# Optimization experiments

Measured on AMD Instinct MI355X. Metric: run time of the kernel, lower is better.

The kernel has to match this reference:

```python
import jax, jax.numpy as jnp
import numpy as np

N, C_IN, C_OUT, H, W = 8, 128, 64, 128, 128
KH, KW, DILATE = 9, 9, 2


def _shifted(xp, dh, dw, dilate, Hh, Ww):
    # xp: zero-padded [N,C,H+2ph,W+2pw]; returns window-offset (dh,dw) view [N,C,H,W]
    return xp[:, :, dh * dilate:dh * dilate + Hh, dw * dilate:dw * dilate + Ww]


def local_similar(q, k, kH, kW, dilate):
    # q,k: [N,C,H,W] -> logits [N,H,W,kH*kW]
    n, c, h, w = q.shape
    ph, pw = dilate * (kH // 2), dilate * (kW // 2)
    kp = jnp.pad(k, ((0, 0), (0, 0), (ph, ph), (pw, pw)))
    outs = []
    for dh in range(kH):
        for dw in range(kW):
            ks = _shifted(kp, dh, dw, dilate, h, w)
            outs.append(jnp.einsum('nchw,nchw->nhw', q, ks))
    return jnp.stack(outs, axis=-1)


def local_weighting(v, wgt, kH, kW, dilate):
    # v: [N,C,H,W], wgt: [N,H,W,kH*kW] -> [N,C,H,W]
    n, c, h, w = v.shape
    ph, pw = dilate * (kH // 2), dilate * (kW // 2)
    vp = jnp.pad(v, ((0, 0), (0, 0), (ph, ph), (pw, pw)))
    out = jnp.zeros_like(v)
    idx = 0
    for dh in range(kH):
        for dw in range(kW):
            vs = _shifted(vp, dh, dw, dilate, h, w)
            out = out + vs * wgt[..., idx][:, None, :, :]
            idx += 1
    return out


def setup_inputs() -> dict:
    key = jax.random.key(0)
    kx, k1, k2, k3 = jax.random.split(key, 4)
    s = 1.0 / np.sqrt(C_IN)
    return {
        'x': jax.random.normal(kx, (N, C_IN, H, W), dtype=jnp.float32),
        'W1': jax.random.normal(k1, (C_OUT, C_IN), dtype=jnp.float32) * s,
        'W2': jax.random.normal(k2, (C_OUT, C_IN), dtype=jnp.float32) * s,
        'W3': jax.random.normal(k3, (C_OUT, C_IN), dtype=jnp.float32) * s,
    }


def reference(x, W1, W2, W3):
    # 1x1 convs (no bias)
    x1 = jnp.einsum('oc,nchw->nohw', W1, x)
    x2 = jnp.einsum('oc,nchw->nohw', W2, x)
    x3 = jnp.einsum('oc,nchw->nohw', W3, x)
    logits = local_similar(x1, x2, KH, KW, DILATE)      # [N,H,W,kH*kW]
    weight = jax.nn.softmax(logits, axis=-1)
    out = local_weighting(x3, weight, KH, KW, DILATE)   # [N,C_out,H,W]
    return out
```

## Files before the change

### kernel.cpp

```cpp
#include <hip/hip_runtime.h>
#include <hip/hip_bf16.h>
#include <cstdint>
#include <cstddef>

#define NB   8
#define CIN  128
#define COUT 64
#define HH   128
#define WWD  128
#define NPIX (NB*HH*WWD)
#define PLANE NPIX
#define LOG2E 1.44269504088896340736f

typedef _Float16 f16;
typedef _Float16 half4_t __attribute__((ext_vector_type(4)));
typedef _Float16 half8_t __attribute__((ext_vector_type(8)));
typedef float    float4_t __attribute__((ext_vector_type(4)));

__global__ __launch_bounds__(256) void wsetup_k(
    const float* __restrict__ W1, const float* __restrict__ W2,
    const float* __restrict__ W3, f16* __restrict__ Wf)
{
  int idx = blockIdx.x * 256 + threadIdx.x;
  int mat = idx >> 13;
  int rem = idx & 8191;
  const float* src = (mat == 0 ? W1 : (mat == 1 ? W2 : W3));
  float v = src[rem];
  if (mat == 0) v *= LOG2E;
  Wf[idx] = (f16)v;
}

__global__ __launch_bounds__(256, 4) void conv_mfma_k(
    const float* __restrict__ x, const f16* __restrict__ Wf,
    f16* __restrict__ Qi, f16* __restrict__ Ki, f16* __restrict__ V2)
{
  __shared__ __align__(16) f16 xs[64 * 136];

  int tid = threadIdx.x, lane = tid & 63, wv = tid >> 6;
  int pxt = blockIdx.x * 64;
  int n = pxt >> 14, hwt = pxt & 16383;

  {
    const float* xp = x + ((size_t)(n * CIN + wv * 32) << 14) + hwt + lane;
    #pragma unroll
    for (int c0 = 0; c0 < 32; c0 += 8) {
      half8_t hh;
      #pragma unroll
      for (int j = 0; j < 8; ++j)
        hh[j] = (f16)xp[(size_t)(c0 + j) << 14];
      *(half8_t*)&xs[lane * 136 + wv * 32 + c0] = hh;
    }
  }
  __syncthreads();

  int l15 = lane & 15, q4 = lane >> 4;

  half8_t wq[4], wk[4], wvf[4];
  #pragma unroll
  for (int k0 = 0; k0 < 4; ++k0) {
    wq[k0]  = *(const half8_t*)&Wf[((wv     )*16 + l15)*128 + k0*32 + q4*8];
    wk[k0]  = *(const half8_t*)&Wf[((wv +  4)*16 + l15)*128 + k0*32 + q4*8];
    wvf[k0] = *(const half8_t*)&Wf[((wv +  8)*16 + l15)*128 + k0*32 + q4*8];
  }

  #pragma unroll
  for (int mt = 0; mt < 4; ++mt) {
    float4_t cq = {0.f,0.f,0.f,0.f}, ck = {0.f,0.f,0.f,0.f}, cv = {0.f,0.f,0.f,0.f};
    #pragma unroll
    for (int k0 = 0; k0 < 4; ++k0) {
      half8_t xa = *(half8_t*)&xs[(mt*16 + l15)*136 + k0*32 + q4*8];
      cq = __builtin_amdgcn_mfma_f32_16x16x32_f16(wq[k0],  xa, cq, 0, 0, 0);
      ck = __builtin_amdgcn_mfma_f32_16x16x32_f16(wk[k0],  xa, ck, 0, 0, 0);
      cv = __builtin_amdgcn_mfma_f32_16x16x32_f16(xa, wvf[k0], cv, 0, 0, 0);
    }
    int pxq = pxt + mt*16 + l15;
    int g   = wv*2 + (q4 >> 1);
    half4_t hq = {(f16)cq[0], (f16)cq[1], (f16)cq[2], (f16)cq[3]};
    half4_t hk = {(f16)ck[0], (f16)ck[1], (f16)ck[2], (f16)ck[3]};
    *(half4_t*)&Qi[((size_t)g * PLANE + pxq) * 8 + (q4 & 1)*4] = hq;
    *(half4_t*)&Ki[((size_t)g * PLANE + pxq) * 8 + (q4 & 1)*4] = hk;
    half4_t hv = {(f16)cv[0], (f16)cv[1], (f16)cv[2], (f16)cv[3]};
    *(half4_t*)&V2[(size_t)(wv*16 + l15) * PLANE + pxt + mt*16 + q4*4] = hv;
  }
}

__global__ __launch_bounds__(512, 4) void attn_fused_k(
    const f16* __restrict__ Qi, const f16* __restrict__ Ki,
    const f16* __restrict__ V2, float* __restrict__ out)
{
  __shared__ __align__(16) f16 plds[8][2][16 * 40];

  int tid = threadIdx.x, lane = tid & 63, wv = tid >> 6;
  int l15 = lane & 15, q4 = lane >> 4;
  int b = blockIdx.x;
  int n = b & 7;
  int p = b >> 3;
  int h0 = (p >> 1)*4 + (p & 1);
  int h2 = h0 + 2;
  int seg = wv * 16;
  int nb = n << 14;

  f16* P0 = &plds[wv][0][0];
  f16* P1 = &plds[wv][1][0];

  half8_t aq0[2], aq1[2];
  {
    int px0 = nb + (h0 << 7) + seg + l15;
    aq0[0] = *(const half8_t*)&Qi[((size_t)(q4    ) * PLANE + px0) * 8];
    aq0[1] = *(const half8_t*)&Qi[((size_t)(q4 + 4) * PLANE + px0) * 8];
    int px1 = px0 + 256;
    aq1[0] = *(const half8_t*)&Qi[((size_t)(q4    ) * PLANE + px1) * 8];
    aq1[1] = *(const half8_t*)&Qi[((size_t)(q4 + 4) * PLANE + px1) * 8];
  }

  unsigned vbits = 0;
  #pragma unroll
  for (int jt = 0; jt < 2; ++jt)
    #pragma unroll
    for (int r = 0; r < 4; ++r) {
      int jw = seg - 8 + jt*16 + q4*4 + r;
      int iw = seg + l15;
      int d  = jw - iw;
      bool val = (((d & 1) == 0) & (d >= -8) & (d <= 8) & ((unsigned)jw < 128u));
      vbits |= ((unsigned)val) << (jt*4 + r);
    }

  float m0 = -1e30f, s0 = 0.f, m1 = -1e30f, s1 = 0.f;
  float4_t o0[4], o1[4];
  #pragma unroll
  for (int ct = 0; ct < 4; ++ct) {
    o0[ct] = (float4_t){0.f,0.f,0.f,0.f};
    o1[ct] = (float4_t){0.f,0.f,0.f,0.f};
  }

  auto row_body = [&](const half8_t* aq, float& m, float& l,
                      float4_t* o, f16* P, const half8_t (&bk)[2][2],
                      const half8_t (&bv)[4]) {
    float4_t st0 = (float4_t){0.f,0.f,0.f,0.f};
    float4_t st1 = (float4_t){0.f,0.f,0.f,0.f};
    st0 = __builtin_amdgcn_mfma_f32_16x16x32_f16(bk[0][0], aq[0], st0, 0, 0, 0);
    st0 = __builtin_amdgcn_mfma_f32_16x16x32_f16(bk[0][1], aq[1], st0, 0, 0, 0);
    st1 = __builtin_amdgcn_mfma_f32_16x16x32_f16(bk[1][0], aq[0], st1, 0, 0, 0);
    st1 = __builtin_amdgcn_mfma_f32_16x16x32_f16(bk[1][1], aq[1], st1, 0, 0, 0);
    #pragma unroll
    for (int r = 0; r < 4; ++r) {
      st0[r] = ((vbits >> r)       & 1u) ? st0[r] : -1e30f;
      st1[r] = ((vbits >> (4 + r)) & 1u) ? st1[r] : -1e30f;
    }
    float v = fmaxf(fmaxf(fmaxf(st0[0], st0[1]), fmaxf(st0[2], st0[3])),
                    fmaxf(fmaxf(st1[0], st1[1]), fmaxf(st1[2], st1[3])));
    v = fmaxf(v, __shfl_xor(v, 16, 64));
    v = fmaxf(v, __shfl_xor(v, 32, 64));
    float mn = fmaxf(m, v);
    float al = exp2f(m - mn);
    m = mn;
    #pragma unroll
    for (int r = 0; r < 4; ++r) {
      st0[r] = exp2f(st0[r] - mn);
      st1[r] = exp2f(st1[r] - mn);
    }
    float rs = (st0[0] + st0[1]) + (st0[2] + st0[3])
             + (st1[0] + st1[1]) + (st1[2] + st1[3]);
    rs += __shfl_xor(rs, 16, 64);
    rs += __shfl_xor(rs, 32, 64);
    l = l * al + rs;
    float4_t alv;
    #pragma unroll
    for (int r = 0; r < 4; ++r) alv[r] = __shfl(al, q4*4 + r, 64);
    #pragma unroll
    for (int ct = 0; ct < 4; ++ct)
      #pragma unroll
      for (int r = 0; r < 4; ++r) o[ct][r] *= alv[r];
    half4_t p0 = {(f16)st0[0], (f16)st0[1], (f16)st0[2], (f16)st0[3]};
    half4_t p1 = {(f16)st1[0], (f16)st1[1], (f16)st1[2], (f16)st1[3]};
    *(half4_t*)&P[l15*40      + q4*4] = p0;
    *(half4_t*)&P[l15*40 + 16 + q4*4] = p1;
    half8_t ap = *(half8_t*)&P[l15*40 + q4*8];
    #pragma unroll
    for (int ct = 0; ct < 4; ++ct)
      o[ct] = __builtin_amdgcn_mfma_f32_16x16x32_f16(ap, bv[ct], o[ct], 0, 0, 0);
  };

  for (int hs = h0 - 8; hs <= h0 + 10; hs += 2) {
    if (hs < 0 || hs > 127) continue;
    bool a0 = (hs <= h0 + 8);
    bool a1 = (hs >= h0 - 6);
    int jbase = nb + (hs << 7) + seg - 8;

    half8_t bk[2][2];
    #pragma unroll
    for (int jt = 0; jt < 2; ++jt) {
      int pxj = jbase + jt*16 + l15;
      bk[jt][0] = *(const half8_t*)&Ki[((size_t)(q4    ) * PLANE + pxj) * 8];
      bk[jt][1] = *(const half8_t*)&Ki[((size_t)(q4 + 4) * PLANE + pxj) * 8];
    }
    half8_t bv[4];
    #pragma unroll
    for (int ct = 0; ct < 4; ++ct)
      bv[ct] = *(const half8_t*)&V2[(size_t)(ct*16 + l15) * PLANE + jbase + q4*8];

    if (a0) row_body(aq0, m0, s0, o0, P0, bk, bv);
    if (a1) row_body(aq1, m1, s1, o1, P1, bk, bv);
  }

  int iw = seg + l15;
  int wlo = iw - 8; if (wlo < 0) wlo = 0;
  int whi = iw + 8; if (whi > 127) whi = 127;
  int vw = ((whi - wlo) >> 1) + 1;
  #pragma unroll
  for (int row = 0; row < 2; ++row) {
    int hr = row ? h2 : h0;
    int hlo = hr - 8; if (hlo < 0) hlo = 0;
    int hhi = hr + 8; if (hhi > 127) hhi = 127;
    int vh = ((hhi - hlo) >> 1) + 1;
    float cnt = (float)(81 - vh * vw);
    float m = row ? m1 : m0, l = row ? s1 : s0;
    float mn = fmaxf(m, 0.f);
    float em = exp2f(m - mn);
    float sc = em / (l * em + cnt * exp2f(-mn));
    float4_t scv;
    #pragma unroll
    for (int r = 0; r < 4; ++r) scv[r] = __shfl(sc, q4*4 + r, 64);
    const float4_t* o = row ? o1 : o0;
    #pragma unroll
    for (int ct = 0; ct < 4; ++ct) {
      size_t ob = ((size_t)(n*COUT + ct*16 + l15) << 14) + (hr << 7) + seg + q4*4;
      float4_t stv;
      #pragma unroll
      for (int r = 0; r < 4; ++r) stv[r] = o[ct][r] * scv[r];
      *(float4_t*)&out[ob] = stv;
    }
  }
}

extern "C" void kernel_launch(void* const* d_in, const int* in_sizes, int n_in,
                              void* d_out, int out_size, void* d_ws, size_t ws_size,
                              hipStream_t stream)
{
  const float* x  = (const float*)d_in[0];
  const float* W1 = (const float*)d_in[1];
  const float* W2 = (const float*)d_in[2];
  const float* W3 = (const float*)d_in[3];

  f16* Wf = (f16*)d_ws;
  f16* Qi = Wf + (size_t)192 * 128;
  f16* Ki = Qi + (size_t)8 * PLANE * 8;
  f16* V2 = Ki + (size_t)8 * PLANE * 8;

  float* outp = (float*)d_out;

  wsetup_k    <<<96,       256, 0, stream>>>(W1, W2, W3, Wf);
  conv_mfma_k <<<NPIX/64,  256, 0, stream>>>(x, Wf, Qi, Ki, V2);
  attn_fused_k<<<NB*HH/2,  512, 0, stream>>>(Qi, Ki, V2, outp);
}
```

Measured before the change: 159.0 us.

## Fuse weight setup into conv, double-buffer K/V loads, split attention blocks

Removes the separate weight conversion kernel; each conv block now reads the fp32 weights and converts them to fp16 in registers, overlapping that with the x tile load. The attention kernel moves from 512-thread to 256-thread blocks covering half a row width each, which doubles the grid to 1024 blocks. It also double-buffers the K/V row loads so the next row's loads are issued before the current row's MFMA and softmax work. Conv blocks are remapped so consecutive blocks interleave images. The cost is redundant weight conversion in every conv block, more register pressure from the double buffers, and a lower occupancy hint.

```diff
diff --git a/kernel.cpp b/kernel.cpp
--- a/kernel.cpp
+++ b/kernel.cpp
@@ -6,9 +6,7 @@
 #define NB   8
 #define CIN  128
 #define COUT 64
-#define HH   128
-#define WWD  128
-#define NPIX (NB*HH*WWD)
+#define NPIX 131072
 #define PLANE NPIX
 #define LOG2E 1.44269504088896340736f
 
@@ -17,28 +15,18 @@
 typedef _Float16 half8_t __attribute__((ext_vector_type(8)));
 typedef float    float4_t __attribute__((ext_vector_type(4)));
 
-__global__ __launch_bounds__(256) void wsetup_k(
-    const float* __restrict__ W1, const float* __restrict__ W2,
-    const float* __restrict__ W3, f16* __restrict__ Wf)
-{
-  int idx = blockIdx.x * 256 + threadIdx.x;
-  int mat = idx >> 13;
-  int rem = idx & 8191;
-  const float* src = (mat == 0 ? W1 : (mat == 1 ? W2 : W3));
-  float v = src[rem];
-  if (mat == 0) v *= LOG2E;
-  Wf[idx] = (f16)v;
-}
-
 __global__ __launch_bounds__(256, 4) void conv_mfma_k(
-    const float* __restrict__ x, const f16* __restrict__ Wf,
+    const float* __restrict__ x,  const float* __restrict__ W1,
+    const float* __restrict__ W2, const float* __restrict__ W3,
     f16* __restrict__ Qi, f16* __restrict__ Ki, f16* __restrict__ V2)
 {
   __shared__ __align__(16) f16 xs[64 * 136];
 
   int tid = threadIdx.x, lane = tid & 63, wv = tid >> 6;
-  int pxt = blockIdx.x * 64;
-  int n = pxt >> 14, hwt = pxt & 16383;
+  int b = blockIdx.x;
+  int n = b & 7, t = b >> 3;
+  int pxt = (n << 14) + t * 64;
+  int hwt = pxt & 16383;
 
   {
     const float* xp = x + ((size_t)(n * CIN + wv * 32) << 14) + hwt + lane;
@@ -51,17 +39,25 @@
       *(half8_t*)&xs[lane * 136 + wv * 32 + c0] = hh;
     }
   }
+
+  int l15 = lane & 15, q4 = lane >> 4;
+
+  half8_t wq[4], wk[4], wvf[4];
+  {
+    const float* r1 = W1 + (wv*16 + l15)*128 + q4*8;
+    const float* r2 = W2 + (wv*16 + l15)*128 + q4*8;
+    const float* r3 = W3 + (wv*16 + l15)*128 + q4*8;
+    #pragma unroll
+    for (int k0 = 0; k0 < 4; ++k0) {
+      #pragma unroll
+      for (int j = 0; j < 8; ++j) {
+        wq[k0][j]  = (f16)(r1[k0*32 + j] * LOG2E);
+        wk[k0][j]  = (f16)(r2[k0*32 + j]);
+        wvf[k0][j] = (f16)(r3[k0*32 + j]);
+      }
+    }
+  }
   __syncthreads();
-
-  int l15 = lane & 15, q4 = lane >> 4;
-
-  half8_t wq[4], wk[4], wvf[4];
-  #pragma unroll
-  for (int k0 = 0; k0 < 4; ++k0) {
-    wq[k0]  = *(const half8_t*)&Wf[((wv     )*16 + l15)*128 + k0*32 + q4*8];
-    wk[k0]  = *(const half8_t*)&Wf[((wv +  4)*16 + l15)*128 + k0*32 + q4*8];
-    wvf[k0] = *(const half8_t*)&Wf[((wv +  8)*16 + l15)*128 + k0*32 + q4*8];
-  }
 
   #pragma unroll
   for (int mt = 0; mt < 4; ++mt) {
@@ -84,20 +80,21 @@
   }
 }
 
-__global__ __launch_bounds__(512, 4) void attn_fused_k(
+__global__ __launch_bounds__(256, 3) void attn_fused_k(
     const f16* __restrict__ Qi, const f16* __restrict__ Ki,
     const f16* __restrict__ V2, float* __restrict__ out)
 {
-  __shared__ __align__(16) f16 plds[8][2][16 * 40];
+  __shared__ __align__(16) f16 plds[4][2][16 * 40];
 
   int tid = threadIdx.x, lane = tid & 63, wv = tid >> 6;
   int l15 = lane & 15, q4 = lane >> 4;
   int b = blockIdx.x;
   int n = b & 7;
-  int p = b >> 3;
+  int r = b >> 3;
+  int p = r & 63, hseg = r >> 6;
   int h0 = (p >> 1)*4 + (p & 1);
   int h2 = h0 + 2;
-  int seg = wv * 16;
+  int seg = (hseg*4 + wv) * 16;
   int nb = n << 14;
 
   f16* P0 = &plds[wv][0][0];
@@ -117,12 +114,12 @@
   #pragma unroll
   for (int jt = 0; jt < 2; ++jt)
     #pragma unroll
-    for (int r = 0; r < 4; ++r) {
-      int jw = seg - 8 + jt*16 + q4*4 + r;
+    for (int rr = 0; rr < 4; ++rr) {
+      int jw = seg - 8 + jt*16 + q4*4 + rr;
       int iw = seg + l15;
       int d  = jw - iw;
       bool val = (((d & 1) == 0) & (d >= -8) & (d <= 8) & ((unsigned)jw < 128u));
-      vbits |= ((unsigned)val) << (jt*4 + r);
+      vbits |= ((unsigned)val) << (jt*4 + rr);
     }
 
   float m0 = -1e30f, s0 = 0.f, m1 = -1e30f, s1 = 0.f;
@@ -143,9 +140,9 @@
     st1 = __builtin_amdgcn_mfma_f32_16x16x32_f16(bk[1][0], aq[0], st1, 0, 0, 0);
     st1 = __builtin_amdgcn_mfma_f32_16x16x32_f16(bk[1][1], aq[1], st1, 0, 0, 0);
     #pragma unroll
-    for (int r = 0; r < 4; ++r) {
-      st0[r] = ((vbits >> r)       & 1u) ? st0[r] : -1e30f;
-      st1[r] = ((vbits >> (4 + r)) & 1u) ? st1[r] : -1e30f;
+    for (int rr = 0; rr < 4; ++rr) {
+      st0[rr] = ((vbits >> rr)       & 1u) ? st0[rr] : -1e30f;
+      st1[rr] = ((vbits >> (4 + rr)) & 1u) ? st1[rr] : -1e30f;
     }
     float v = fmaxf(fmaxf(fmaxf(st0[0], st0[1]), fmaxf(st0[2], st0[3])),
                     fmaxf(fmaxf(st1[0], st1[1]), fmaxf(st1[2], st1[3])));
@@ -155,9 +152,9 @@
     float al = exp2f(m - mn);
     m = mn;
     #pragma unroll
-    for (int r = 0; r < 4; ++r) {
-      st0[r] = exp2f(st0[r] - mn);
-      st1[r] = exp2f(st1[r] - mn);
+    for (int rr = 0; rr < 4; ++rr) {
+      st0[rr] = exp2f(st0[rr] - mn);
+      st1[rr] = exp2f(st1[rr] - mn);
     }
     float rs = (st0[0] + st0[1]) + (st0[2] + st0[3])
              + (st1[0] + st1[1]) + (st1[2] + st1[3]);
@@ -166,11 +163,11 @@
     l = l * al + rs;
     float4_t alv;
     #pragma unroll
-    for (int r = 0; r < 4; ++r) alv[r] = __shfl(al, q4*4 + r, 64);
+    for (int rr = 0; rr < 4; ++rr) alv[rr] = __shfl(al, q4*4 + rr, 64);
     #pragma unroll
     for (int ct = 0; ct < 4; ++ct)
       #pragma unroll
-      for (int r = 0; r < 4; ++r) o[ct][r] *= alv[r];
+      for (int rr = 0; rr < 4; ++rr) o[ct][rr] *= alv[rr];
     half4_t p0 = {(f16)st0[0], (f16)st0[1], (f16)st0[2], (f16)st0[3]};
     half4_t p1 = {(f16)st1[0], (f16)st1[1], (f16)st1[2], (f16)st1[3]};
     *(half4_t*)&P[l15*40      + q4*4] = p0;
@@ -181,26 +178,37 @@
       o[ct] = __builtin_amdgcn_mfma_f32_16x16x32_f16(ap, bv[ct], o[ct], 0, 0, 0);
   };
 
-  for (int hs = h0 - 8; hs <= h0 + 10; hs += 2) {
-    if (hs < 0 || hs > 127) continue;
-    bool a0 = (hs <= h0 + 8);
-    bool a1 = (hs >= h0 - 6);
+  auto loadKV = [&](int hs, half8_t (&bk)[2][2], half8_t (&bv)[4]) {
     int jbase = nb + (hs << 7) + seg - 8;
-
-    half8_t bk[2][2];
     #pragma unroll
     for (int jt = 0; jt < 2; ++jt) {
       int pxj = jbase + jt*16 + l15;
       bk[jt][0] = *(const half8_t*)&Ki[((size_t)(q4    ) * PLANE + pxj) * 8];
       bk[jt][1] = *(const half8_t*)&Ki[((size_t)(q4 + 4) * PLANE + pxj) * 8];
     }
-    half8_t bv[4];
     #pragma unroll
     for (int ct = 0; ct < 4; ++ct)
       bv[ct] = *(const half8_t*)&V2[(size_t)(ct*16 + l15) * PLANE + jbase + q4*8];
-
-    if (a0) row_body(aq0, m0, s0, o0, P0, bk, bv);
-    if (a1) row_body(aq1, m1, s1, o1, P1, bk, bv);
+  };
+
+  auto process = [&](int hs, const half8_t (&bk)[2][2], const half8_t (&bv)[4]) {
+    if (hs <= h0 + 8) row_body(aq0, m0, s0, o0, P0, bk, bv);
+    if (hs >= h2 - 8) row_body(aq1, m1, s1, o1, P1, bk, bv);
+  };
+
+  int hs_lo = h0 - 8;  if (hs_lo < 0)   hs_lo = h0 & 1;
+  int hs_hi = h0 + 10; if (hs_hi > 127) hs_hi = 126 + (h0 & 1);
+
+  half8_t bkA[2][2], bvA[4], bkB[2][2], bvB[4];
+  loadKV(hs_lo, bkA, bvA);
+  int hs = hs_lo;
+  while (true) {
+    if (hs + 2 <= hs_hi) loadKV(hs + 2, bkB, bvB);
+    process(hs, bkA, bvA);
+    hs += 2; if (hs > hs_hi) break;
+    if (hs + 2 <= hs_hi) loadKV(hs + 2, bkA, bvA);
+    process(hs, bkB, bvB);
+    hs += 2; if (hs > hs_hi) break;
   }
 
   int iw = seg + l15;
@@ -220,14 +228,14 @@
     float sc = em / (l * em + cnt * exp2f(-mn));
     float4_t scv;
     #pragma unroll
-    for (int r = 0; r < 4; ++r) scv[r] = __shfl(sc, q4*4 + r, 64);
+    for (int rr = 0; rr < 4; ++rr) scv[rr] = __shfl(sc, q4*4 + rr, 64);
     const float4_t* o = row ? o1 : o0;
     #pragma unroll
     for (int ct = 0; ct < 4; ++ct) {
       size_t ob = ((size_t)(n*COUT + ct*16 + l15) << 14) + (hr << 7) + seg + q4*4;
       float4_t stv;
       #pragma unroll
-      for (int r = 0; r < 4; ++r) stv[r] = o[ct][r] * scv[r];
+      for (int rr = 0; rr < 4; ++rr) stv[rr] = o[ct][rr] * scv[rr];
       *(float4_t*)&out[ob] = stv;
     }
   }
@@ -242,14 +250,12 @@
   const float* W2 = (const float*)d_in[2];
   const float* W3 = (const float*)d_in[3];
 
-  f16* Wf = (f16*)d_ws;
-  f16* Qi = Wf + (size_t)192 * 128;
+  f16* Qi = (f16*)d_ws + 2048;
   f16* Ki = Qi + (size_t)8 * PLANE * 8;
   f16* V2 = Ki + (size_t)8 * PLANE * 8;
 
   float* outp = (float*)d_out;
 
-  wsetup_k    <<<96,       256, 0, stream>>>(W1, W2, W3, Wf);
-  conv_mfma_k <<<NPIX/64,  256, 0, stream>>>(x, Wf, Qi, Ki, V2);
-  attn_fused_k<<<NB*HH/2,  512, 0, stream>>>(Qi, Ki, V2, outp);
+  conv_mfma_k <<<NPIX/64, 256, 0, stream>>>(x, W1, W2, W3, Qi, Ki, V2);
+  attn_fused_k<<<1024,    256, 0, stream>>>(Qi, Ki, V2, outp);
 }
```

New measurement: 176.0 us. 10.7% more time.

## Drop online-softmax max tracking and switch P and V to bf16 MFMA

Applied to the files above, without the earlier changes.

Removes the running-max and rescale steps of the online softmax. Raw logits are exponentiated directly, and each lane keeps a partial row sum that is shuffle-reduced once at the end. P and V are stored as bf16, with P truncated from the fp32 bits, so the unshifted exponentials fit in bf16's fp32-like exponent range, and the PV product uses the bf16 MFMA. This cuts per-tile shuffles, max reductions and accumulator rescaling. In exchange it can overflow if logits ever exceed about 128 in log2 units, and it loses mantissa precision in P and V.

```diff
diff --git a/kernel.cpp b/kernel.cpp
--- a/kernel.cpp
+++ b/kernel.cpp
@@ -6,16 +6,21 @@
 #define NB   8
 #define CIN  128
 #define COUT 64
-#define HH   128
-#define WWD  128
-#define NPIX (NB*HH*WWD)
+#define NPIX 131072
 #define PLANE NPIX
 #define LOG2E 1.44269504088896340736f
 
 typedef _Float16 f16;
 typedef _Float16 half4_t __attribute__((ext_vector_type(4)));
 typedef _Float16 half8_t __attribute__((ext_vector_type(8)));
+typedef short    bs8    __attribute__((ext_vector_type(8)));
 typedef float    float4_t __attribute__((ext_vector_type(4)));
+typedef unsigned int uint2_t __attribute__((ext_vector_type(2)));
+
+__device__ __forceinline__ unsigned short f2bf(float f){
+  unsigned u = __float_as_uint(f);
+  return (unsigned short)((u + 0x7fffu + ((u >> 16) & 1u)) >> 16);
+}
 
 __global__ __launch_bounds__(256) void wsetup_k(
     const float* __restrict__ W1, const float* __restrict__ W2,
@@ -32,7 +37,7 @@
 
 __global__ __launch_bounds__(256, 4) void conv_mfma_k(
     const float* __restrict__ x, const f16* __restrict__ Wf,
-    f16* __restrict__ Qi, f16* __restrict__ Ki, f16* __restrict__ V2)
+    f16* __restrict__ Qi, f16* __restrict__ Ki, unsigned short* __restrict__ V2)
 {
   __shared__ __align__(16) f16 xs[64 * 136];
 
@@ -79,16 +84,18 @@
     half4_t hk = {(f16)ck[0], (f16)ck[1], (f16)ck[2], (f16)ck[3]};
     *(half4_t*)&Qi[((size_t)g * PLANE + pxq) * 8 + (q4 & 1)*4] = hq;
     *(half4_t*)&Ki[((size_t)g * PLANE + pxq) * 8 + (q4 & 1)*4] = hk;
-    half4_t hv = {(f16)cv[0], (f16)cv[1], (f16)cv[2], (f16)cv[3]};
-    *(half4_t*)&V2[(size_t)(wv*16 + l15) * PLANE + pxt + mt*16 + q4*4] = hv;
+    uint2_t pv;
+    pv.x = (unsigned)f2bf(cv[0]) | ((unsigned)f2bf(cv[1]) << 16);
+    pv.y = (unsigned)f2bf(cv[2]) | ((unsigned)f2bf(cv[3]) << 16);
+    *(uint2_t*)&V2[(size_t)(wv*16 + l15) * PLANE + pxt + mt*16 + q4*4] = pv;
   }
 }
 
 __global__ __launch_bounds__(512, 4) void attn_fused_k(
     const f16* __restrict__ Qi, const f16* __restrict__ Ki,
-    const f16* __restrict__ V2, float* __restrict__ out)
-{
-  __shared__ __align__(16) f16 plds[8][2][16 * 40];
+    const unsigned short* __restrict__ V2, float* __restrict__ out)
+{
+  __shared__ __align__(16) unsigned short plds[8][2][16 * 40];
 
   int tid = threadIdx.x, lane = tid & 63, wv = tid >> 6;
   int l15 = lane & 15, q4 = lane >> 4;
@@ -100,8 +107,8 @@
   int seg = wv * 16;
   int nb = n << 14;
 
-  f16* P0 = &plds[wv][0][0];
-  f16* P1 = &plds[wv][1][0];
+  unsigned short* P0 = &plds[wv][0][0];
+  unsigned short* P1 = &plds[wv][1][0];
 
   half8_t aq0[2], aq1[2];
   {
@@ -117,15 +124,15 @@
   #pragma unroll
   for (int jt = 0; jt < 2; ++jt)
     #pragma unroll
-    for (int r = 0; r < 4; ++r) {
-      int jw = seg - 8 + jt*16 + q4*4 + r;
+    for (int rr = 0; rr < 4; ++rr) {
+      int jw = seg - 8 + jt*16 + q4*4 + rr;
       int iw = seg + l15;
       int d  = jw - iw;
       bool val = (((d & 1) == 0) & (d >= -8) & (d <= 8) & ((unsigned)jw < 128u));
-      vbits |= ((unsigned)val) << (jt*4 + r);
-    }
-
-  float m0 = -1e30f, s0 = 0.f, m1 = -1e30f, s1 = 0.f;
+      vbits |= ((unsigned)val) << (jt*4 + rr);
+    }
+
+  float s0 = 0.f, s1 = 0.f;
   float4_t o0[4], o1[4];
   #pragma unroll
   for (int ct = 0; ct < 4; ++ct) {
@@ -133,9 +140,9 @@
     o1[ct] = (float4_t){0.f,0.f,0.f,0.f};
   }
 
-  auto row_body = [&](const half8_t* aq, float& m, float& l,
-                      float4_t* o, f16* P, const half8_t (&bk)[2][2],
-                      const half8_t (&bv)[4]) {
+  auto row_body = [&](const half8_t* aq, float& s_part,
+                      float4_t* o, unsigned short* P,
+                      const half8_t (&bk)[2][2], const bs8 (&bv)[4]) {
     float4_t st0 = (float4_t){0.f,0.f,0.f,0.f};
     float4_t st1 = (float4_t){0.f,0.f,0.f,0.f};
     st0 = __builtin_amdgcn_mfma_f32_16x16x32_f16(bk[0][0], aq[0], st0, 0, 0, 0);
@@ -143,48 +150,27 @@
     st1 = __builtin_amdgcn_mfma_f32_16x16x32_f16(bk[1][0], aq[0], st1, 0, 0, 0);
     st1 = __builtin_amdgcn_mfma_f32_16x16x32_f16(bk[1][1], aq[1], st1, 0, 0, 0);
     #pragma unroll
-    for (int r = 0; r < 4; ++r) {
-      st0[r] = ((vbits >> r)       & 1u) ? st0[r] : -1e30f;
-      st1[r] = ((vbits >> (4 + r)) & 1u) ? st1[r] : -1e30f;
-    }
-    float v = fmaxf(fmaxf(fmaxf(st0[0], st0[1]), fmaxf(st0[2], st0[3])),
-                    fmaxf(fmaxf(st1[0], st1[1]), fmaxf(st1[2], st1[3])));
-    v = fmaxf(v, __shfl_xor(v, 16, 64));
-    v = fmaxf(v, __shfl_xor(v, 32, 64));
-    float mn = fmaxf(m, v);
-    float al = exp2f(m - mn);
-    m = mn;
-    #pragma unroll
-    for (int r = 0; r < 4; ++r) {
-      st0[r] = exp2f(st0[r] - mn);
-      st1[r] = exp2f(st1[r] - mn);
-    }
-    float rs = (st0[0] + st0[1]) + (st0[2] + st0[3])
-             + (st1[0] + st1[1]) + (st1[2] + st1[3]);
-    rs += __shfl_xor(rs, 16, 64);
-    rs += __shfl_xor(rs, 32, 64);
-    l = l * al + rs;
-    float4_t alv;
-    #pragma unroll
-    for (int r = 0; r < 4; ++r) alv[r] = __shfl(al, q4*4 + r, 64);
+    for (int rr = 0; rr < 4; ++rr) {
+      st0[rr] = exp2f(((vbits >> rr)       & 1u) ? st0[rr] : -1e30f);
+      st1[rr] = exp2f(((vbits >> (4 + rr)) & 1u) ? st1[rr] : -1e30f);
+    }
+    s_part += (st0[0] + st0[1]) + (st0[2] + st0[3])
+            + (st1[0] + st1[1]) + (st1[2] + st1[3]);
+    uint2_t pk0, pk1;
+    pk0.x = (__float_as_uint(st0[1]) & 0xffff0000u) | (__float_as_uint(st0[0]) >> 16);
+    pk0.y = (__float_as_uint(st0[3]) & 0xffff0000u) | (__float_as_uint(st0[2]) >> 16);
+    pk1.x = (__float_as_uint(st1[1]) & 0xffff0000u) | (__float_as_uint(st1[0]) >> 16);
+    pk1.y = (__float_as_uint(st1[3]) & 0xffff0000u) | (__float_as_uint(st1[2]) >> 16);
+    *(uint2_t*)&P[l15*40      + q4*4] = pk0;
+    *(uint2_t*)&P[l15*40 + 16 + q4*4] = pk1;
+    bs8 ap = *(bs8*)&P[l15*40 + q4*8];
     #pragma unroll
     for (int ct = 0; ct < 4; ++ct)
-      #pragma unroll
-      for (int r = 0; r < 4; ++r) o[ct][r] *= alv[r];
-    half4_t p0 = {(f16)st0[0], (f16)st0[1], (f16)st0[2], (f16)st0[3]};
-    half4_t p1 = {(f16)st1[0], (f16)st1[1], (f16)st1[2], (f16)st1[3]};
-    *(half4_t*)&P[l15*40      + q4*4] = p0;
-    *(half4_t*)&P[l15*40 + 16 + q4*4] = p1;
-    half8_t ap = *(half8_t*)&P[l15*40 + q4*8];
-    #pragma unroll
-    for (int ct = 0; ct < 4; ++ct)
-      o[ct] = __builtin_amdgcn_mfma_f32_16x16x32_f16(ap, bv[ct], o[ct], 0, 0, 0);
+      o[ct] = __builtin_amdgcn_mfma_f32_16x16x32_bf16(ap, bv[ct], o[ct], 0, 0, 0);
   };
 
   for (int hs = h0 - 8; hs <= h0 + 10; hs += 2) {
     if (hs < 0 || hs > 127) continue;
-    bool a0 = (hs <= h0 + 8);
-    bool a1 = (hs >= h0 - 6);
     int jbase = nb + (hs << 7) + seg - 8;
 
     half8_t bk[2][2];
@@ -194,13 +180,13 @@
       bk[jt][0] = *(const half8_t*)&Ki[((size_t)(q4    ) * PLANE + pxj) * 8];
       bk[jt][1] = *(const half8_t*)&Ki[((size_t)(q4 + 4) * PLANE + pxj) * 8];
     }
-    half8_t bv[4];
+    bs8 bv[4];
     #pragma unroll
     for (int ct = 0; ct < 4; ++ct)
-      bv[ct] = *(const half8_t*)&V2[(size_t)(ct*16 + l15) * PLANE + jbase + q4*8];
-
-    if (a0) row_body(aq0, m0, s0, o0, P0, bk, bv);
-    if (a1) row_body(aq1, m1, s1, o1, P1, bk, bv);
+      bv[ct] = *(const bs8*)&V2[(size_t)(ct*16 + l15) * PLANE + jbase + q4*8];
+
+    if (hs <= h0 + 8) row_body(aq0, s0, o0, P0, bk, bv);
+    if (hs >= h2 - 8) row_body(aq1, s1, o1, P1, bk, bv);
   }
 
   int iw = seg + l15;
@@ -214,20 +200,20 @@
     int hhi = hr + 8; if (hhi > 127) hhi = 127;
     int vh = ((hhi - hlo) >> 1) + 1;
     float cnt = (float)(81 - vh * vw);
-    float m = row ? m1 : m0, l = row ? s1 : s0;
-    float mn = fmaxf(m, 0.f);
-    float em = exp2f(m - mn);
-    float sc = em / (l * em + cnt * exp2f(-mn));
+    float srow = row ? s1 : s0;
+    srow += __shfl_xor(srow, 16, 64);
+    srow += __shfl_xor(srow, 32, 64);
+    float sc = 1.f / (srow + cnt);
     float4_t scv;
     #pragma unroll
-    for (int r = 0; r < 4; ++r) scv[r] = __shfl(sc, q4*4 + r, 64);
+    for (int rr = 0; rr < 4; ++rr) scv[rr] = __shfl(sc, q4*4 + rr, 64);
     const float4_t* o = row ? o1 : o0;
     #pragma unroll
     for (int ct = 0; ct < 4; ++ct) {
       size_t ob = ((size_t)(n*COUT + ct*16 + l15) << 14) + (hr << 7) + seg + q4*4;
       float4_t stv;
       #pragma unroll
-      for (int r = 0; r < 4; ++r) stv[r] = o[ct][r] * scv[r];
+      for (int rr = 0; rr < 4; ++rr) stv[rr] = o[ct][rr] * scv[rr];
       *(float4_t*)&out[ob] = stv;
     }
   }
@@ -245,11 +231,11 @@
   f16* Wf = (f16*)d_ws;
   f16* Qi = Wf + (size_t)192 * 128;
   f16* Ki = Qi + (size_t)8 * PLANE * 8;
-  f16* V2 = Ki + (size_t)8 * PLANE * 8;
+  unsigned short* V2 = (unsigned short*)(Ki + (size_t)8 * PLANE * 8);
 
   float* outp = (float*)d_out;
 
   wsetup_k    <<<96,       256, 0, stream>>>(W1, W2, W3, Wf);
   conv_mfma_k <<<NPIX/64,  256, 0, stream>>>(x, Wf, Qi, Ki, V2);
-  attn_fused_k<<<NB*HH/2,  512, 0, stream>>>(Qi, Ki, V2, outp);
-}
+  attn_fused_k<<<NB*128/2, 512, 0, stream>>>(Qi, Ki, V2, outp);
+}
```

New measurement: 157.9 us. Within noise of the previous version (-0.7%).
